# Kernel tuning notes

Measured on AMD Instinct MI355X. Metric: run time of the kernel, lower is better.

The kernel has to match this reference:

```python
import jax, jax.numpy as jnp
import numpy as np

EMBED_DIM = 256
MIN_SCALE = 0.5
BASE = 100.0
NDIM = 3
EPS = 1e-5


def basis_norm(psi, w):
    # w: [B, N] float weights; reduce over token dim (-2)
    norm_sq = jnp.sum(w[..., None] * (psi * psi), axis=-2, keepdims=True)
    return psi / jnp.sqrt(norm_sq + EPS)


def rotary(f, coords, lift):
    # lift: [D//2, 3]; phase: [B, N, D//2]
    phase = coords @ lift.T
    c, s = jnp.cos(phase), jnp.sin(phase)
    f1, f2 = jnp.split(f, 2, axis=-1)
    return jnp.concatenate([f1 * c - f2 * s, f1 * s + f2 * c], axis=-1)


def setup_inputs() -> dict:
    key = jax.random.key(0)
    ks = jax.random.split(key, 12)
    B, N, D = 4, 8192, EMBED_DIM
    phi = jax.random.normal(ks[0], (B, N, D), dtype=jnp.float32)
    coords = jax.random.normal(ks[1], (B, N, NDIM), dtype=jnp.float32)
    weights = jax.random.uniform(ks[2], (B, N), dtype=jnp.float32)
    scale = 1.0 / np.sqrt(D)
    Wq = jax.random.normal(ks[3], (D, D), dtype=jnp.float32) * scale
    bq = jnp.zeros((D,), dtype=jnp.float32)
    Wk = jax.random.normal(ks[4], (D, D), dtype=jnp.float32) * scale
    bk = jax.random.normal(ks[5], (D,), dtype=jnp.float32) * 0.01
    Wv = jax.random.normal(ks[6], (D, D), dtype=jnp.float32) * scale
    bv = jax.random.normal(ks[7], (D,), dtype=jnp.float32) * 0.01
    Wo = jax.random.normal(ks[8], (D, D), dtype=jnp.float32) * scale
    bo = jnp.zeros((D,), dtype=jnp.float32)
    # rotary lift init: k_norms * random unit vecs
    half = D // 2
    scales = BASE ** (-2.0 * np.arange(half) / D)
    k_norms = (2.0 * np.pi / MIN_SCALE) * scales  # [half]
    u = np.asarray(jax.random.normal(ks[9], (half, NDIM)))
    u = u / np.linalg.norm(u, axis=-1, keepdims=True)
    lift = jnp.asarray(k_norms[:, None] * u, dtype=jnp.float32)  # [half, 3]
    return {"phi": phi, "coords": coords, "weights": weights,
            "Wq": Wq, "bq": bq, "Wk": Wk, "bk": bk, "Wv": Wv, "bv": bv,
            "Wo": Wo, "bo": bo, "lift": lift}


def reference(phi, coords, weights, Wq, bq, Wk, bk, Wv, bv, Wo, bo, lift):
    q = phi @ Wq.T + bq
    k = basis_norm(phi @ Wk.T + bk, weights)
    v = basis_norm(phi @ Wv.T + bv, weights)
    q = rotary(q, coords, lift)
    k = rotary(k, coords, lift)
    k = k * weights[..., None]  # float-weights branch
    kv = jnp.einsum('bnd,bne->bde', k, v)   # [B, D, D]
    out = jnp.einsum('bnd,bde->bne', q, kv)  # [B, N, D]
    return out @ Wo.T + bo
```

## Files before the change

kernel.cpp:

```cpp
#include <hip/hip_runtime.h>
#include <hip/hip_bf16.h>
#include <stdint.h>

#define DEV __device__ __forceinline__

typedef short short8 __attribute__((ext_vector_type(8)));
typedef float floatx4 __attribute__((ext_vector_type(4)));

constexpr int D = 256;
constexpr int NTOK = 8192;
constexpr int MTOT = 4 * NTOK;

DEV void gl_lds16(const void* g, void* l) {
  __builtin_amdgcn_global_load_lds(
      (const __attribute__((address_space(1))) void*)g,
      (__attribute__((address_space(3))) void*)l, 16, 0, 0);
}

DEV float bflo(uint32_t u) { return __uint_as_float(u << 16); }
DEV float bfhi(uint32_t u) { return __uint_as_float(u & 0xffff0000u); }
DEV uint32_t packbf(float a, float b) {
  uint16_t xa = __builtin_bit_cast(uint16_t, __float2bfloat16(a));
  uint16_t xb = __builtin_bit_cast(uint16_t, __float2bfloat16(b));
  return (uint32_t)xa | ((uint32_t)xb << 16);
}

constexpr int PHI_E = MTOT * D;
constexpr int W_E = D * D;
__global__ __launch_bounds__(256) void convert(
    const float* __restrict__ phi, const float* __restrict__ Wq,
    const float* __restrict__ Wk, const float* __restrict__ Wv,
    uint32_t* __restrict__ dst) {
  const int idx2 = blockIdx.x * 256 + threadIdx.x;
  const int e0 = idx2 * 2;
  float2 v;
  if (e0 < PHI_E) {
    v = ((const float2*)phi)[idx2];
  } else {
    int r = e0 - PHI_E;
    if (r < W_E) v = ((const float2*)Wq)[r >> 1];
    else if (r < 2 * W_E) v = ((const float2*)Wk)[(r - W_E) >> 1];
    else v = ((const float2*)Wv)[(r - 2 * W_E) >> 1];
  }
  dst[idx2] = packbf(v.x, v.y);
}

__global__ __launch_bounds__(256, 2) void gemm_qkv(
    const __hip_bfloat16* __restrict__ phi,
    const __hip_bfloat16* __restrict__ W16,
    const float* __restrict__ bq, const float* __restrict__ bk, const float* __restrict__ bv,
    const float* __restrict__ coords, const float* __restrict__ wts,
    const float* __restrict__ lift,
    __hip_bfloat16* __restrict__ Qb, __hip_bfloat16* __restrict__ Kb,
    __hip_bfloat16* __restrict__ Vb, float* __restrict__ nsk, float* __restrict__ nsv) {
  __shared__ __align__(16) char As[8192];
  __shared__ __align__(16) char Bs[16384];
  const int t = threadIdx.x, lane = t & 63, wid = t >> 6;
  const int wm = (wid & 1) * 64, wn = (wid >> 1) * 64;
  const int l16 = lane & 15, q4 = lane >> 4;
  const int m0 = blockIdx.x * 128;
  const int mat = blockIdx.y;
  const __hip_bfloat16* W = W16 + (size_t)mat * W_E;
  const float* bias = (mat == 0) ? bq : (mat == 1) ? bk : bv;
  __hip_bfloat16* Out = (mat == 0) ? Qb : (mat == 1) ? Kb : Vb;

  floatx4 acc[4][8] = {};

  const int srow = wid * 16 + (lane >> 2);
  const int skoff = (lane & 3) * 8;
  const __hip_bfloat16* gA = phi + (size_t)(m0 + srow) * D + skoff;
  const __hip_bfloat16* gB = W + (size_t)srow * D + skoff;
  char* lA = As + srow * 64 + skoff * 2;
  char* lB = Bs + srow * 64 + skoff * 2;

  for (int kt = 0; kt < 256; kt += 32) {
    gl_lds16(gA + kt, lA);
    gl_lds16(gA + kt + 64 * D, lA + 4096);
    gl_lds16(gB + kt, lB);
    gl_lds16(gB + kt + 64 * D, lB + 4096);
    gl_lds16(gB + kt + 128 * D, lB + 8192);
    gl_lds16(gB + kt + 192 * D, lB + 12288);
    __syncthreads();
    short8 af[4], bf8[8];
#pragma unroll
    for (int i = 0; i < 4; i++)
      af[i] = *(const short8*)(As + (wm + i * 16 + l16) * 64 + q4 * 16);
#pragma unroll
    for (int j = 0; j < 8; j++) {
      const int col = wn + (j & 3) * 16 + (j >> 2) * 128 + l16;
      bf8[j] = *(const short8*)(Bs + col * 64 + q4 * 16);
    }
#pragma unroll
    for (int i = 0; i < 4; i++)
#pragma unroll
      for (int j = 0; j < 8; j++)
        acc[i][j] = __builtin_amdgcn_mfma_f32_16x16x32_bf16(af[i], bf8[j], acc[i][j], 0, 0, 0);
    __syncthreads();
  }

  float bcol[8];
#pragma unroll
  for (int j = 0; j < 8; j++)
    bcol[j] = bias[wn + (j & 3) * 16 + (j >> 2) * 128 + l16];

  if (mat == 0) {
    float lx[4], ly[4], lz[4];
#pragma unroll
    for (int jj = 0; jj < 4; jj++) {
      const int c = wn + jj * 16 + l16;
      lx[jj] = lift[c * 3 + 0]; ly[jj] = lift[c * 3 + 1]; lz[jj] = lift[c * 3 + 2];
    }
#pragma unroll
    for (int i = 0; i < 4; i++) {
#pragma unroll
      for (int r = 0; r < 4; r++) {
        const int row = m0 + wm + i * 16 + q4 * 4 + r;
        const float cx = coords[row * 3 + 0];
        const float cy = coords[row * 3 + 1];
        const float cz = coords[row * 3 + 2];
#pragma unroll
        for (int jj = 0; jj < 4; jj++) {
          const int c = wn + jj * 16 + l16;
          const float p = cx * lx[jj] + cy * ly[jj] + cz * lz[jj];
          float s, cs;
          __sincosf(p, &s, &cs);
          const float f1 = acc[i][jj][r] + bcol[jj];
          const float f2 = acc[i][jj + 4][r] + bcol[jj + 4];
          Out[(size_t)row * D + c]       = __float2bfloat16(f1 * cs - f2 * s);
          Out[(size_t)row * D + c + 128] = __float2bfloat16(f1 * s + f2 * cs);
        }
      }
    }
  } else {
    const int b = m0 >> 13;
    float* ns = (mat == 1) ? nsk : nsv;
    float colsum[8] = {};
#pragma unroll
    for (int i = 0; i < 4; i++) {
#pragma unroll
      for (int r = 0; r < 4; r++) {
        const int row = m0 + wm + i * 16 + q4 * 4 + r;
        const float w = wts[row];
#pragma unroll
        for (int j = 0; j < 8; j++) {
          const int col = wn + (j & 3) * 16 + (j >> 2) * 128 + l16;
          const float psi = acc[i][j][r] + bcol[j];
          Out[(size_t)row * D + col] = __float2bfloat16(psi);
          colsum[j] += w * psi * psi;
        }
      }
    }
#pragma unroll
    for (int j = 0; j < 8; j++) {
      float s = colsum[j];
      s += __shfl_xor(s, 16);
      s += __shfl_xor(s, 32);
      if (q4 == 0) {
        const int col = wn + (j & 3) * 16 + (j >> 2) * 128 + l16;
        atomicAdd(&ns[b * D + col], s);
      }
    }
  }
}

__global__ __launch_bounds__(256) void pointwise_k(
    __hip_bfloat16* __restrict__ Kb, const float* __restrict__ coords,
    const float* __restrict__ wts, const float* __restrict__ lift,
    const float* __restrict__ nsk) {
  const int t = threadIdx.x;
  const int j = t & 63, rloc = t >> 6;
  const size_t row = (size_t)blockIdx.x * 4 + rloc;
  const int b = (int)(row >> 13);
  const float cx = coords[row * 3 + 0];
  const float cy = coords[row * 3 + 1];
  const float cz = coords[row * 3 + 2];
  const int j0 = 2 * j, j1 = 2 * j + 1;
  const float p0 = cx * lift[j0 * 3 + 0] + cy * lift[j0 * 3 + 1] + cz * lift[j0 * 3 + 2];
  const float p1 = cx * lift[j1 * 3 + 0] + cy * lift[j1 * 3 + 1] + cz * lift[j1 * 3 + 2];
  float s0, c0, s1, c1;
  __sincosf(p0, &s0, &c0);
  __sincosf(p1, &s1, &c1);
  const float w = wts[row];
  uint32_t* K32 = (uint32_t*)Kb;
  const size_t base = row * 128;
  const int nb = b * D;
  const float ik0 = rsqrtf(nsk[nb + j0] + 1e-5f);
  const float ik1 = rsqrtf(nsk[nb + j1] + 1e-5f);
  const float ik2 = rsqrtf(nsk[nb + 128 + j0] + 1e-5f);
  const float ik3 = rsqrtf(nsk[nb + 128 + j1] + 1e-5f);
  const uint32_t klo = K32[base + j], khi = K32[base + 64 + j];
  const float k1a = bflo(klo) * ik0, k1b = bfhi(klo) * ik1;
  const float k2a = bflo(khi) * ik2, k2b = bfhi(khi) * ik3;
  K32[base + j]      = packbf((k1a * c0 - k2a * s0) * w, (k1b * c1 - k2b * s1) * w);
  K32[base + 64 + j] = packbf((k1a * s0 + k2a * c0) * w, (k1b * s1 + k2b * c1) * w);
}

__global__ __launch_bounds__(256) void make_wosv(
    const float* __restrict__ Wo, const float* __restrict__ nsv,
    uint32_t* __restrict__ wosv) {
  const int b = blockIdx.x >> 7;
  const int f = (blockIdx.x & 127) * 2 + (threadIdx.x >> 7);
  const int e2 = threadIdx.x & 127;
  const float2 wo = ((const float2*)(Wo + (size_t)f * D))[e2];
  const float2 nv = ((const float2*)(nsv + b * D))[e2];
  const float a = wo.x * rsqrtf(nv.x + 1e-5f);
  const float c = wo.y * rsqrtf(nv.y + 1e-5f);
  wosv[(size_t)b * 32768 + f * 128 + e2] = packbf(a, c);
}

__global__ __launch_bounds__(256, 2) void gemm_vproj(
    const __hip_bfloat16* __restrict__ A, const __hip_bfloat16* __restrict__ Wsv,
    __hip_bfloat16* __restrict__ Og) {
  __shared__ __align__(16) char As[8192];
  __shared__ __align__(16) char Bs[8192];
  const int t = threadIdx.x, lane = t & 63, wid = t >> 6;
  const int wm = (wid & 1) * 64, wn = (wid >> 1) * 64;
  const int l16 = lane & 15, q4 = lane >> 4;
  const int m0 = blockIdx.x * 128, n0 = blockIdx.y * 128;
  const int b = m0 >> 13;
  const __hip_bfloat16* W = Wsv + ((size_t)b << 16);
  floatx4 acc[4][4] = {};
  const int srow = wid * 16 + (lane >> 2);
  const int skoff = (lane & 3) * 8;
  const __hip_bfloat16* gA = A + (size_t)(m0 + srow) * D + skoff;
  const __hip_bfloat16* gB = W + (size_t)(n0 + srow) * D + skoff;
  char* lA = As + srow * 64 + skoff * 2;
  char* lB = Bs + srow * 64 + skoff * 2;
  for (int kt = 0; kt < 256; kt += 32) {
    gl_lds16(gA + kt, lA);
    gl_lds16(gA + kt + 64 * D, lA + 4096);
    gl_lds16(gB + kt, lB);
    gl_lds16(gB + kt + 64 * D, lB + 4096);
    __syncthreads();
    short8 af[4], bf8[4];
#pragma unroll
    for (int i = 0; i < 4; i++) {
      af[i]  = *(const short8*)(As + (wm + i * 16 + l16) * 64 + q4 * 16);
      bf8[i] = *(const short8*)(Bs + (wn + i * 16 + l16) * 64 + q4 * 16);
    }
#pragma unroll
    for (int i = 0; i < 4; i++)
#pragma unroll
      for (int j = 0; j < 4; j++)
        acc[i][j] = __builtin_amdgcn_mfma_f32_16x16x32_bf16(af[i], bf8[j], acc[i][j], 0, 0, 0);
    __syncthreads();
  }
#pragma unroll
  for (int j = 0; j < 4; j++) {
    const int colg = n0 + wn + j * 16 + l16;
#pragma unroll
    for (int i = 0; i < 4; i++) {
      const int rowg = m0 + wm + i * 16 + q4 * 4;
#pragma unroll
      for (int r = 0; r < 4; r++)
        Og[(size_t)(rowg + r) * D + colg] = __float2bfloat16(acc[i][j][r]);
    }
  }
}

__global__ __launch_bounds__(256, 2) void gemm_tn(
    const __hip_bfloat16* __restrict__ Vp, const __hip_bfloat16* __restrict__ Kwb,
    float* __restrict__ KVt) {
  __shared__ __align__(16) char sm[2 * 32 * 260];
  char* Asm = sm;
  char* Bsm = sm + 32 * 260;
  const int t = threadIdx.x, lane = t & 63, wid = t >> 6;
  const int wm = (wid & 1) * 64, wn = (wid >> 1) * 64;
  const int l16 = lane & 15, q4 = lane >> 4;
  const int chunk = blockIdx.x;
  const int ed = blockIdx.y, b = blockIdx.z;
  const int e0 = (ed & 1) * 128, d0 = (ed >> 1) * 128;
  const uint32_t* V32 = (const uint32_t*)Vp;
  const uint32_t* K32 = (const uint32_t*)Kwb;
  floatx4 acc[4][4] = {};
  for (int nt = 0; nt < 512; nt += 32) {
    const int nbase = chunk * 512 + nt;
#pragma unroll
    for (int rep = 0; rep < 8; rep++) {
      const int flat = rep * 256 + t;
      const int nn = flat >> 6;
      const int e2 = flat & 63;
      const size_t src = ((size_t)b * NTOK + nbase + nn) * 128;
      *(uint32_t*)(Asm + nn * 260 + e2 * 4) = V32[src + (e0 >> 1) + e2];
      *(uint32_t*)(Bsm + nn * 260 + e2 * 4) = K32[src + (d0 >> 1) + e2];
    }
    __syncthreads();
    short8 af[4], bf8[4];
#pragma unroll
    for (int i = 0; i < 4; i++) {
#pragma unroll
      for (int jj = 0; jj < 8; jj++) {
        af[i][jj]  = *(const short*)(Asm + (q4 * 8 + jj) * 260 + (wm + i * 16 + l16) * 2);
        bf8[i][jj] = *(const short*)(Bsm + (q4 * 8 + jj) * 260 + (wn + i * 16 + l16) * 2);
      }
    }
#pragma unroll
    for (int i = 0; i < 4; i++)
#pragma unroll
      for (int j = 0; j < 4; j++)
        acc[i][j] = __builtin_amdgcn_mfma_f32_16x16x32_bf16(af[i], bf8[j], acc[i][j], 0, 0, 0);
    __syncthreads();
  }
#pragma unroll
  for (int i = 0; i < 4; i++) {
#pragma unroll
    for (int r = 0; r < 4; r++) {
      const int eg = e0 + wm + i * 16 + q4 * 4 + r;
#pragma unroll
      for (int j = 0; j < 4; j++) {
        const int dg = d0 + wn + j * 16 + l16;
        atomicAdd(&KVt[((size_t)b * D + eg) * D + dg], acc[i][j][r]);
      }
    }
  }
}

__global__ __launch_bounds__(256) void kvt2bf(const float* __restrict__ KVt,
                                              uint32_t* __restrict__ P) {
  const int idx = blockIdx.x * 256 + threadIdx.x;
  const float2 v = ((const float2*)KVt)[idx];
  P[idx] = packbf(v.x, v.y);
}

__global__ __launch_bounds__(256, 2) void gemm_out(
    const __hip_bfloat16* __restrict__ A, const __hip_bfloat16* __restrict__ Pm,
    const float* __restrict__ bo, float* __restrict__ Og) {
  __shared__ __align__(16) char As[8192];
  __shared__ __align__(16) char Bs[8192];
  const int t = threadIdx.x, lane = t & 63, wid = t >> 6;
  const int wm = (wid & 1) * 64, wn = (wid >> 1) * 64;
  const int l16 = lane & 15, q4 = lane >> 4;
  const int m0 = blockIdx.x * 128, n0 = blockIdx.y * 128;
  const int b = m0 >> 13;
  const __hip_bfloat16* W = Pm + ((size_t)b << 16);
  floatx4 acc[4][4] = {};
  const int srow = wid * 16 + (lane >> 2);
  const int skoff = (lane & 3) * 8;
  const __hip_bfloat16* gA = A + (size_t)(m0 + srow) * D + skoff;
  const __hip_bfloat16* gB = W + (size_t)(n0 + srow) * D + skoff;
  char* lA = As + srow * 64 + skoff * 2;
  char* lB = Bs + srow * 64 + skoff * 2;
  for (int kt = 0; kt < 256; kt += 32) {
    gl_lds16(gA + kt, lA);
    gl_lds16(gA + kt + 64 * D, lA + 4096);
    gl_lds16(gB + kt, lB);
    gl_lds16(gB + kt + 64 * D, lB + 4096);
    __syncthreads();
    short8 af[4], bf8[4];
#pragma unroll
    for (int i = 0; i < 4; i++) {
      af[i]  = *(const short8*)(As + (wm + i * 16 + l16) * 64 + q4 * 16);
      bf8[i] = *(const short8*)(Bs + (wn + i * 16 + l16) * 64 + q4 * 16);
    }
#pragma unroll
    for (int i = 0; i < 4; i++)
#pragma unroll
      for (int j = 0; j < 4; j++)
        acc[i][j] = __builtin_amdgcn_mfma_f32_16x16x32_bf16(af[i], bf8[j], acc[i][j], 0, 0, 0);
    __syncthreads();
  }
#pragma unroll
  for (int j = 0; j < 4; j++) {
    const int colg = n0 + wn + j * 16 + l16;
    const float bb = bo[colg];
#pragma unroll
    for (int i = 0; i < 4; i++) {
      const int rowg = m0 + wm + i * 16 + q4 * 4;
#pragma unroll
      for (int r = 0; r < 4; r++)
        Og[(size_t)(rowg + r) * D + colg] = acc[i][j][r] + bb;
    }
  }
}

extern "C" void kernel_launch(void* const* d_in, const int* in_sizes, int n_in,
                              void* d_out, int out_size, void* d_ws, size_t ws_size,
                              hipStream_t stream) {
  const float* phi    = (const float*)d_in[0];
  const float* coords = (const float*)d_in[1];
  const float* wts    = (const float*)d_in[2];
  const float* bq     = (const float*)d_in[4];
  const float* bk     = (const float*)d_in[6];
  const float* bv     = (const float*)d_in[8];
  const float* Wo     = (const float*)d_in[9];
  const float* bo     = (const float*)d_in[10];
  const float* lift   = (const float*)d_in[11];

  char* ws = (char*)d_ws;
  __hip_bfloat16* phi16 = (__hip_bfloat16*)ws;
  __hip_bfloat16* W16   = (__hip_bfloat16*)(ws + 16777216);
  const size_t QOFF = 17170432;
  const size_t SZ = (size_t)MTOT * D * 2;
  __hip_bfloat16* Qb = (__hip_bfloat16*)(ws + QOFF);
  __hip_bfloat16* Kb = (__hip_bfloat16*)(ws + QOFF + SZ);
  __hip_bfloat16* Vb = (__hip_bfloat16*)(ws + QOFF + 2 * SZ);
  const size_t NOFF = QOFF + 3 * SZ;
  float* nsk = (float*)(ws + NOFF);
  float* nsv = (float*)(ws + NOFF + 4096);
  float* KVt = (float*)(ws + NOFF + 8192);
  __hip_bfloat16* P    = (__hip_bfloat16*)(ws + NOFF + 8192 + 1048576);
  __hip_bfloat16* wosv = (__hip_bfloat16*)(ws + NOFF + 8192 + 1048576 + 524288);
  __hip_bfloat16* vproj = (__hip_bfloat16*)(ws + NOFF + 8192 + 1048576 + 2 * 524288);

  hipMemsetAsync(ws + NOFF, 0, 8192 + 1048576, stream);

  convert<<<16768, 256, 0, stream>>>(phi, (const float*)d_in[3], (const float*)d_in[5],
                                     (const float*)d_in[7], (uint32_t*)ws);
  gemm_qkv<<<dim3(256, 3), 256, 0, stream>>>(phi16, W16, bq, bk, bv, coords, wts, lift,
                                             Qb, Kb, Vb, nsk, nsv);
  pointwise_k<<<8192, 256, 0, stream>>>(Kb, coords, wts, lift, nsk);
  make_wosv<<<512, 256, 0, stream>>>(Wo, nsv, (uint32_t*)wosv);
  gemm_vproj<<<dim3(256, 2), 256, 0, stream>>>(Vb, wosv, vproj);
  gemm_tn<<<dim3(16, 4, 4), 256, 0, stream>>>(vproj, Kb, KVt);
  kvt2bf<<<512, 256, 0, stream>>>(KVt, (uint32_t*)P);
  gemm_out<<<dim3(256, 2), 256, 0, stream>>>(Qb, P, bo, (float*)d_out);
}
```

Baseline: 205.1 us.

## Fuse K rotary, Wo scaling and V projection into one launch; replace atomics with split-K partials

```diff
diff --git a/kernel.cpp b/kernel.cpp
--- a/kernel.cpp
+++ b/kernel.cpp
@@ -6,6 +6,7 @@
 
 typedef short short8 __attribute__((ext_vector_type(8)));
 typedef float floatx4 __attribute__((ext_vector_type(4)));
+typedef uint32_t uint32x4 __attribute__((ext_vector_type(4)));
 
 constexpr int D = 256;
 constexpr int NTOK = 8192;
@@ -163,104 +164,117 @@
   }
 }
 
-__global__ __launch_bounds__(256) void pointwise_k(
+__global__ __launch_bounds__(256, 2) void vproj_pk(
+    const __hip_bfloat16* __restrict__ Vb, const float* __restrict__ Wo,
+    const float* __restrict__ nsv, __hip_bfloat16* __restrict__ vproj,
     __hip_bfloat16* __restrict__ Kb, const float* __restrict__ coords,
     const float* __restrict__ wts, const float* __restrict__ lift,
     const float* __restrict__ nsk) {
-  const int t = threadIdx.x;
-  const int j = t & 63, rloc = t >> 6;
-  const size_t row = (size_t)blockIdx.x * 4 + rloc;
-  const int b = (int)(row >> 13);
-  const float cx = coords[row * 3 + 0];
-  const float cy = coords[row * 3 + 1];
-  const float cz = coords[row * 3 + 2];
-  const int j0 = 2 * j, j1 = 2 * j + 1;
-  const float p0 = cx * lift[j0 * 3 + 0] + cy * lift[j0 * 3 + 1] + cz * lift[j0 * 3 + 2];
-  const float p1 = cx * lift[j1 * 3 + 0] + cy * lift[j1 * 3 + 1] + cz * lift[j1 * 3 + 2];
-  float s0, c0, s1, c1;
-  __sincosf(p0, &s0, &c0);
-  __sincosf(p1, &s1, &c1);
-  const float w = wts[row];
-  uint32_t* K32 = (uint32_t*)Kb;
-  const size_t base = row * 128;
-  const int nb = b * D;
-  const float ik0 = rsqrtf(nsk[nb + j0] + 1e-5f);
-  const float ik1 = rsqrtf(nsk[nb + j1] + 1e-5f);
-  const float ik2 = rsqrtf(nsk[nb + 128 + j0] + 1e-5f);
-  const float ik3 = rsqrtf(nsk[nb + 128 + j1] + 1e-5f);
-  const uint32_t klo = K32[base + j], khi = K32[base + 64 + j];
-  const float k1a = bflo(klo) * ik0, k1b = bfhi(klo) * ik1;
-  const float k2a = bflo(khi) * ik2, k2b = bfhi(khi) * ik3;
-  K32[base + j]      = packbf((k1a * c0 - k2a * s0) * w, (k1b * c1 - k2b * s1) * w);
-  K32[base + 64 + j] = packbf((k1a * s0 + k2a * c0) * w, (k1b * s1 + k2b * c1) * w);
-}
-
-__global__ __launch_bounds__(256) void make_wosv(
-    const float* __restrict__ Wo, const float* __restrict__ nsv,
-    uint32_t* __restrict__ wosv) {
-  const int b = blockIdx.x >> 7;
-  const int f = (blockIdx.x & 127) * 2 + (threadIdx.x >> 7);
-  const int e2 = threadIdx.x & 127;
-  const float2 wo = ((const float2*)(Wo + (size_t)f * D))[e2];
-  const float2 nv = ((const float2*)(nsv + b * D))[e2];
-  const float a = wo.x * rsqrtf(nv.x + 1e-5f);
-  const float c = wo.y * rsqrtf(nv.y + 1e-5f);
-  wosv[(size_t)b * 32768 + f * 128 + e2] = packbf(a, c);
-}
-
-__global__ __launch_bounds__(256, 2) void gemm_vproj(
-    const __hip_bfloat16* __restrict__ A, const __hip_bfloat16* __restrict__ Wsv,
-    __hip_bfloat16* __restrict__ Og) {
   __shared__ __align__(16) char As[8192];
   __shared__ __align__(16) char Bs[8192];
-  const int t = threadIdx.x, lane = t & 63, wid = t >> 6;
-  const int wm = (wid & 1) * 64, wn = (wid >> 1) * 64;
-  const int l16 = lane & 15, q4 = lane >> 4;
-  const int m0 = blockIdx.x * 128, n0 = blockIdx.y * 128;
-  const int b = m0 >> 13;
-  const __hip_bfloat16* W = Wsv + ((size_t)b << 16);
-  floatx4 acc[4][4] = {};
-  const int srow = wid * 16 + (lane >> 2);
-  const int skoff = (lane & 3) * 8;
-  const __hip_bfloat16* gA = A + (size_t)(m0 + srow) * D + skoff;
-  const __hip_bfloat16* gB = W + (size_t)(n0 + srow) * D + skoff;
-  char* lA = As + srow * 64 + skoff * 2;
-  char* lB = Bs + srow * 64 + skoff * 2;
-  for (int kt = 0; kt < 256; kt += 32) {
-    gl_lds16(gA + kt, lA);
-    gl_lds16(gA + kt + 64 * D, lA + 4096);
-    gl_lds16(gB + kt, lB);
-    gl_lds16(gB + kt + 64 * D, lB + 4096);
-    __syncthreads();
-    short8 af[4], bf8[4];
-#pragma unroll
-    for (int i = 0; i < 4; i++) {
-      af[i]  = *(const short8*)(As + (wm + i * 16 + l16) * 64 + q4 * 16);
-      bf8[i] = *(const short8*)(Bs + (wn + i * 16 + l16) * 64 + q4 * 16);
-    }
-#pragma unroll
-    for (int i = 0; i < 4; i++)
-#pragma unroll
-      for (int j = 0; j < 4; j++)
-        acc[i][j] = __builtin_amdgcn_mfma_f32_16x16x32_bf16(af[i], bf8[j], acc[i][j], 0, 0, 0);
-    __syncthreads();
-  }
-#pragma unroll
-  for (int j = 0; j < 4; j++) {
-    const int colg = n0 + wn + j * 16 + l16;
-#pragma unroll
-    for (int i = 0; i < 4; i++) {
-      const int rowg = m0 + wm + i * 16 + q4 * 4;
-#pragma unroll
-      for (int r = 0; r < 4; r++)
-        Og[(size_t)(rowg + r) * D + colg] = __float2bfloat16(acc[i][j][r]);
+  __shared__ __align__(16) float isv[256];
+  const int bx = blockIdx.x;
+  const int t = threadIdx.x;
+
+  if (bx < 512) {
+    const int lane = t & 63, wid = t >> 6;
+    const int wm = (wid & 1) * 64, wn = (wid >> 1) * 64;
+    const int l16 = lane & 15, q4 = lane >> 4;
+    const int m0 = (bx >> 1) * 128, n0 = (bx & 1) * 128;
+    const int b = m0 >> 13;
+    isv[t] = rsqrtf(nsv[b * D + t] + 1e-5f);
+    __syncthreads();
+    floatx4 acc[4][4] = {};
+    const int srow = wid * 16 + (lane >> 2);
+    const int skoff = (lane & 3) * 8;
+    const __hip_bfloat16* gA = Vb + (size_t)(m0 + srow) * D + skoff;
+    const float* gB0 = Wo + (size_t)(n0 + srow) * D + skoff;
+    const float* gB1 = Wo + (size_t)(n0 + srow + 64) * D + skoff;
+    char* lA = As + srow * 64 + skoff * 2;
+    char* lB = Bs + srow * 64 + skoff * 2;
+    for (int kt = 0; kt < 256; kt += 32) {
+      gl_lds16(gA + kt, lA);
+      gl_lds16(gA + kt + 64 * D, lA + 4096);
+      const float4 w0 = *(const float4*)(gB0 + kt);
+      const float4 w1 = *(const float4*)(gB0 + kt + 4);
+      const float4 w2 = *(const float4*)(gB1 + kt);
+      const float4 w3 = *(const float4*)(gB1 + kt + 4);
+      const float4 i0 = *(const float4*)(&isv[kt + skoff]);
+      const float4 i1 = *(const float4*)(&isv[kt + skoff + 4]);
+      uint32x4 p0, p1;
+      p0[0] = packbf(w0.x * i0.x, w0.y * i0.y);
+      p0[1] = packbf(w0.z * i0.z, w0.w * i0.w);
+      p0[2] = packbf(w1.x * i1.x, w1.y * i1.y);
+      p0[3] = packbf(w1.z * i1.z, w1.w * i1.w);
+      p1[0] = packbf(w2.x * i0.x, w2.y * i0.y);
+      p1[1] = packbf(w2.z * i0.z, w2.w * i0.w);
+      p1[2] = packbf(w3.x * i1.x, w3.y * i1.y);
+      p1[3] = packbf(w3.z * i1.z, w3.w * i1.w);
+      *(uint32x4*)lB = p0;
+      *(uint32x4*)(lB + 4096) = p1;
+      __syncthreads();
+      short8 af[4], bf8[4];
+#pragma unroll
+      for (int i = 0; i < 4; i++) {
+        af[i]  = *(const short8*)(As + (wm + i * 16 + l16) * 64 + q4 * 16);
+        bf8[i] = *(const short8*)(Bs + (wn + i * 16 + l16) * 64 + q4 * 16);
+      }
+#pragma unroll
+      for (int i = 0; i < 4; i++)
+#pragma unroll
+        for (int j = 0; j < 4; j++)
+          acc[i][j] = __builtin_amdgcn_mfma_f32_16x16x32_bf16(af[i], bf8[j], acc[i][j], 0, 0, 0);
+      __syncthreads();
+    }
+#pragma unroll
+    for (int j = 0; j < 4; j++) {
+      const int colg = n0 + wn + j * 16 + l16;
+#pragma unroll
+      for (int i = 0; i < 4; i++) {
+        const int rowg = m0 + wm + i * 16 + q4 * 4;
+#pragma unroll
+        for (int r = 0; r < 4; r++)
+          vproj[(size_t)(rowg + r) * D + colg] = __float2bfloat16(acc[i][j][r]);
+      }
+    }
+  } else {
+    const int j = t & 63, rloc = t >> 6;
+    const int pb = bx - 512;
+    const int r0 = pb * 256;
+    const int b = r0 >> 13;
+    const int j0 = 2 * j, j1 = 2 * j + 1;
+    const float lx0 = lift[j0 * 3 + 0], ly0 = lift[j0 * 3 + 1], lz0 = lift[j0 * 3 + 2];
+    const float lx1 = lift[j1 * 3 + 0], ly1 = lift[j1 * 3 + 1], lz1 = lift[j1 * 3 + 2];
+    const int nb = b * D;
+    const float ik0 = rsqrtf(nsk[nb + j0] + 1e-5f);
+    const float ik1 = rsqrtf(nsk[nb + j1] + 1e-5f);
+    const float ik2 = rsqrtf(nsk[nb + 128 + j0] + 1e-5f);
+    const float ik3 = rsqrtf(nsk[nb + 128 + j1] + 1e-5f);
+    uint32_t* K32 = (uint32_t*)Kb;
+    for (int it = 0; it < 64; it++) {
+      const size_t row = (size_t)r0 + it * 4 + rloc;
+      const float cx = coords[row * 3 + 0];
+      const float cy = coords[row * 3 + 1];
+      const float cz = coords[row * 3 + 2];
+      const float p0 = cx * lx0 + cy * ly0 + cz * lz0;
+      const float p1 = cx * lx1 + cy * ly1 + cz * lz1;
+      float s0, c0, s1, c1;
+      __sincosf(p0, &s0, &c0);
+      __sincosf(p1, &s1, &c1);
+      const float w = wts[row];
+      const size_t base = row * 128;
+      const uint32_t klo = K32[base + j], khi = K32[base + 64 + j];
+      const float k1a = bflo(klo) * ik0, k1b = bfhi(klo) * ik1;
+      const float k2a = bflo(khi) * ik2, k2b = bfhi(khi) * ik3;
+      K32[base + j]      = packbf((k1a * c0 - k2a * s0) * w, (k1b * c1 - k2b * s1) * w);
+      K32[base + 64 + j] = packbf((k1a * s0 + k2a * c0) * w, (k1b * s1 + k2b * c1) * w);
     }
   }
 }
 
 __global__ __launch_bounds__(256, 2) void gemm_tn(
     const __hip_bfloat16* __restrict__ Vp, const __hip_bfloat16* __restrict__ Kwb,
-    float* __restrict__ KVt) {
+    float* __restrict__ part) {
   __shared__ __align__(16) char sm[2 * 32 * 260];
   char* Asm = sm;
   char* Bsm = sm + 32 * 260;
@@ -273,8 +287,8 @@
   const uint32_t* V32 = (const uint32_t*)Vp;
   const uint32_t* K32 = (const uint32_t*)Kwb;
   floatx4 acc[4][4] = {};
-  for (int nt = 0; nt < 512; nt += 32) {
-    const int nbase = chunk * 512 + nt;
+  for (int nt = 0; nt < 256; nt += 32) {
+    const int nbase = chunk * 256 + nt;
 #pragma unroll
     for (int rep = 0; rep < 8; rep++) {
       const int flat = rep * 256 + t;
@@ -301,6 +315,7 @@
         acc[i][j] = __builtin_amdgcn_mfma_f32_16x16x32_bf16(af[i], bf8[j], acc[i][j], 0, 0, 0);
     __syncthreads();
   }
+  float* pt = part + (((size_t)(chunk * 4 + b)) << 16);
 #pragma unroll
   for (int i = 0; i < 4; i++) {
 #pragma unroll
@@ -309,17 +324,25 @@
 #pragma unroll
       for (int j = 0; j < 4; j++) {
         const int dg = d0 + wn + j * 16 + l16;
-        atomicAdd(&KVt[((size_t)b * D + eg) * D + dg], acc[i][j][r]);
-      }
-    }
-  }
-}
-
-__global__ __launch_bounds__(256) void kvt2bf(const float* __restrict__ KVt,
-                                              uint32_t* __restrict__ P) {
-  const int idx = blockIdx.x * 256 + threadIdx.x;
-  const float2 v = ((const float2*)KVt)[idx];
-  P[idx] = packbf(v.x, v.y);
+        pt[eg * 256 + dg] = acc[i][j][r];
+      }
+    }
+  }
+}
+
+__global__ __launch_bounds__(256) void reduce_kvt(const float* __restrict__ part,
+                                                  uint32_t* __restrict__ P) {
+  const int flat2 = blockIdx.x * 256 + threadIdx.x;
+  const int b = flat2 >> 15;
+  const int off2 = flat2 & 32767;
+  const float2* p2 = (const float2*)part;
+  float sx = 0, sy = 0;
+#pragma unroll
+  for (int c = 0; c < 32; c++) {
+    const float2 v = p2[(((size_t)(c * 4 + b)) << 15) + off2];
+    sx += v.x; sy += v.y;
+  }
+  P[flat2] = packbf(sx, sy);
 }
 
 __global__ __launch_bounds__(256, 2) void gemm_out(
@@ -397,21 +420,18 @@
   const size_t NOFF = QOFF + 3 * SZ;
   float* nsk = (float*)(ws + NOFF);
   float* nsv = (float*)(ws + NOFF + 4096);
-  float* KVt = (float*)(ws + NOFF + 8192);
-  __hip_bfloat16* P    = (__hip_bfloat16*)(ws + NOFF + 8192 + 1048576);
-  __hip_bfloat16* wosv = (__hip_bfloat16*)(ws + NOFF + 8192 + 1048576 + 524288);
-  __hip_bfloat16* vproj = (__hip_bfloat16*)(ws + NOFF + 8192 + 1048576 + 2 * 524288);
-
-  hipMemsetAsync(ws + NOFF, 0, 8192 + 1048576, stream);
+  float* part = (float*)(ws + NOFF + 8192);
+  __hip_bfloat16* P = (__hip_bfloat16*)(ws + NOFF + 8192 + 33554432);
+  __hip_bfloat16* vproj = (__hip_bfloat16*)(ws + NOFF + 8192 + 33554432 + 524288);
+
+  hipMemsetAsync(ws + NOFF, 0, 8192, stream);
 
   convert<<<16768, 256, 0, stream>>>(phi, (const float*)d_in[3], (const float*)d_in[5],
                                      (const float*)d_in[7], (uint32_t*)ws);
   gemm_qkv<<<dim3(256, 3), 256, 0, stream>>>(phi16, W16, bq, bk, bv, coords, wts, lift,
                                              Qb, Kb, Vb, nsk, nsv);
-  pointwise_k<<<8192, 256, 0, stream>>>(Kb, coords, wts, lift, nsk);
-  make_wosv<<<512, 256, 0, stream>>>(Wo, nsv, (uint32_t*)wosv);
-  gemm_vproj<<<dim3(256, 2), 256, 0, stream>>>(Vb, wosv, vproj);
-  gemm_tn<<<dim3(16, 4, 4), 256, 0, stream>>>(vproj, Kb, KVt);
-  kvt2bf<<<512, 256, 0, stream>>>(KVt, (uint32_t*)P);
+  vproj_pk<<<640, 256, 0, stream>>>(Vb, Wo, nsv, vproj, Kb, coords, wts, lift, nsk);
+  gemm_tn<<<dim3(32, 4, 4), 256, 0, stream>>>(vproj, Kb, part);
+  reduce_kvt<<<512, 256, 0, stream>>>(part, (uint32_t*)P);
   gemm_out<<<dim3(256, 2), 256, 0, stream>>>(Qb, P, bo, (float*)d_out);
 }
```

After: 196.1 us. -4.4%, faster.
